# Kernel optimization log

Measured on AMD Instinct MI355X. Metric: run time of the kernel, lower is better.

The kernel has to match this reference:

```python
import jax, jax.numpy as jnp
import numpy as np

ALPHA = 0.9
DT = 0.1


def setup_inputs() -> dict:
    key = jax.random.key(0)
    ks = jax.random.split(key, 9)
    B, N_in, N, L, N_out, T = 256, 784, 1024, 4, 10, 100
    s = 0.05  # small init scale to keep sin() in a sensible regime
    return {
        "X": jax.random.normal(ks[0], (B, N_in), jnp.float32),
        "Wi_w": jax.random.normal(ks[1], (N, N_in), jnp.float32) * s,
        "Wi_b": jax.random.normal(ks[2], (N,), jnp.float32) * s,
        "Win_w": jax.random.normal(ks[3], (L, N, N), jnp.float32) * s,
        "Win_b": jax.random.normal(ks[4], (L, N), jnp.float32) * s,
        "Wrec_w": jax.random.normal(ks[5], (L, N, N), jnp.float32) * s,
        "Wrec_b": jax.random.normal(ks[6], (L, N), jnp.float32) * s,
        "Wo_w": jax.random.normal(ks[7], (N_out, N), jnp.float32) * s,
        "Wo_b": jax.random.normal(ks[8], (N_out,), jnp.float32) * s,
        "T": 100,
    }


def reference(X, Wi_w, Wi_b, Win_w, Win_b, Wrec_w, Wrec_b, Wo_w, Wo_b, T):
    L = Wrec_w.shape[0]
    B = X.shape[0]
    N = Wi_w.shape[0]
    # input projection computed once (as in the original: x_in outside the loop)
    x_in = X.reshape(B, -1) @ Wi_w.T + Wi_b  # [B, N]
    h0 = jnp.zeros((L, B, N), X.dtype)

    def step(h, _):
        hs = []
        # layer 0: dh = -alpha*h + sin(x_in + W_rec0 h)
        h0n = h[0] + DT * (-ALPHA * h[0] + jnp.sin(x_in + h[0] @ Wrec_w[0].T + Wrec_b[0]))
        hs.append(h0n)
        # layers 1..L-1 use the *updated* h of the layer below (matches torch loop order)
        for l in range(1, L):
            pre = hs[l - 1] @ Win_w[l].T + Win_b[l] + h[l] @ Wrec_w[l].T + Wrec_b[l]
            hs.append(h[l] + DT * (-ALPHA * h[l] + jnp.sin(pre)))
        return jnp.stack(hs), None

    hT, _ = jax.lax.scan(step, h0, None, length=T)
    return hT[-1] @ Wo_w.T + Wo_b  # [B, N_out]
```

## Files before the change

kernel.cpp:

```cpp
#include <hip/hip_runtime.h>
#include <hip/hip_fp16.h>

constexpr float ALPHA = 0.9f;
constexpr float DT    = 0.1f;
constexpr int BB   = 256;
constexpr int NIN  = 784;
constexpr int NN   = 1024;
constexpr int LL   = 4;
constexpr int NOUT = 10;
constexpr int TT   = 100;
constexpr int KXP  = 832;
constexpr int NSTAGE = TT + LL - 1;
constexpr unsigned GRIDN = 256;
constexpr unsigned GRPSZ = 32;
constexpr int NC = 32;

typedef _Float16 f16x8 __attribute__((ext_vector_type(8)));
typedef _Float16 f16x4 __attribute__((ext_vector_type(4)));
typedef float    f32x4 __attribute__((ext_vector_type(4)));

#define GLL16(g, l) __builtin_amdgcn_global_load_lds( \
    (const __attribute__((address_space(1))) unsigned int*)(g), \
    (__attribute__((address_space(3))) unsigned int*)(l), 16, 0, 0)

#define VMCNT(n) asm volatile("s_waitcnt vmcnt(" #n ")" ::: "memory")

__global__ void wconv_kernel(const float* __restrict__ Wrec,
                             const float* __restrict__ Win,
                             _Float16* __restrict__ Wrec_h,
                             _Float16* __restrict__ Win_h) {
    size_t i = (size_t)blockIdx.x * blockDim.x + threadIdx.x;
    float4 r = ((const float4*)Wrec)[i];
    float4 n = ((const float4*)Win)[i];
    f16x4 rh = {(_Float16)r.x, (_Float16)r.y, (_Float16)r.z, (_Float16)r.w};
    f16x4 nh = {(_Float16)n.x, (_Float16)n.y, (_Float16)n.z, (_Float16)n.w};
    ((f16x4*)Wrec_h)[i] = rh;
    ((f16x4*)Win_h)[i]  = nh;
}

__global__ void prep_kernel(const float* __restrict__ X,
                            const float* __restrict__ Wi_w,
                            _Float16* __restrict__ Xh_hi, _Float16* __restrict__ Xh_lo,
                            _Float16* __restrict__ Wih_hi, _Float16* __restrict__ Wih_lo) {
    int row = blockIdx.x;
    const float* src;
    _Float16 *dhi, *dlo;
    if (row < BB) {
        src = X + (size_t)row * NIN;
        dhi = Xh_hi + (size_t)row * KXP;  dlo = Xh_lo + (size_t)row * KXP;
    } else {
        int r = row - BB;
        src = Wi_w + (size_t)r * NIN;
        dhi = Wih_hi + (size_t)r * KXP;   dlo = Wih_lo + (size_t)r * KXP;
    }
    for (int k = threadIdx.x; k < KXP; k += 256) {
        float v = (k < NIN) ? src[k] : 0.f;
        _Float16 hi = (_Float16)v;
        dhi[k] = hi;
        dlo[k] = (_Float16)(v - (float)hi);
    }
}

__global__ void bias_kernel(const float* __restrict__ Win_b,
                            const float* __restrict__ Wrec_b,
                            float* __restrict__ bc) {
    int i = blockIdx.x * 256 + threadIdx.x;
    int l = i >> 10;
    float v = Wrec_b[i];
    if (l > 0) v += Win_b[i];
    bc[i] = v;
}

__global__ __launch_bounds__(256, 1) void xin_gemm(
    const _Float16* __restrict__ Xh_hi, const _Float16* __restrict__ Xh_lo,
    const _Float16* __restrict__ Wih_hi, const _Float16* __restrict__ Wih_lo,
    const float* __restrict__ Wi_b, float* __restrict__ x_in) {
    const int b = blockIdx.x;
    const int mt = b & 1, nt = b >> 1;
    const int row0 = mt * 128, col0 = nt * 64;

    const _Float16* Alist[3] = { Xh_hi + (size_t)row0 * KXP, Xh_hi + (size_t)row0 * KXP,
                                 Xh_lo + (size_t)row0 * KXP };
    const _Float16* Blist[3] = { Wih_hi + (size_t)col0 * KXP, Wih_lo + (size_t)col0 * KXP,
                                 Wih_hi + (size_t)col0 * KXP };

    __shared__ __align__(16) _Float16 ldsA[2][128 * 64];
    __shared__ __align__(16) _Float16 ldsB[2][64 * 64];

    const int tid = threadIdx.x;
    const int w = tid >> 6, lane = tid & 63;
    const int lm = lane & 15, kg = lane >> 4;
    const int rsub = lane >> 3, cch = lane & 7;
    const int wr = w >> 1, wc = w & 1;

    f32x4 acc[4][2] = {};
    constexpr int NIT = 3 * (KXP / 64);

    auto stage = [&](int kk, int buf) {
        int p = (kk >= 26) ? 2 : (kk >= 13 ? 1 : 0);
        int kw = (kk - p * 13) * 64;
        const _Float16* Ap = Alist[p];
        const _Float16* Bp = Blist[p];
        #pragma unroll
        for (int i = 0; i < 4; ++i) {
            const _Float16* g = Ap + (size_t)((w * 4 + i) * 8 + rsub) * KXP + kw + ((cch ^ rsub) * 8);
            GLL16(g, &ldsA[buf][(w * 4 + i) * 512]);
        }
        #pragma unroll
        for (int i = 0; i < 2; ++i) {
            const _Float16* g = Bp + (size_t)((w * 2 + i) * 8 + rsub) * KXP + kw + ((cch ^ rsub) * 8);
            GLL16(g, &ldsB[buf][(w * 2 + i) * 512]);
        }
    };

    stage(0, 0);
    __syncthreads();
    for (int kk = 0; kk < NIT; ++kk) {
        int cur = kk & 1;
        if (kk + 1 < NIT) stage(kk + 1, cur ^ 1);
        const _Float16* lA = ldsA[cur];
        const _Float16* lB = ldsB[cur];
        #pragma unroll
        for (int ks = 0; ks < 2; ++ks) {
            f16x8 a[4], bf[2];
            #pragma unroll
            for (int am = 0; am < 4; ++am) {
                int r = wr * 64 + am * 16 + lm;
                a[am] = *(const f16x8*)(lA + r * 64 + ((((ks << 2) | kg) ^ (lm & 7)) * 8));
            }
            #pragma unroll
            for (int bn = 0; bn < 2; ++bn) {
                int c = wc * 32 + bn * 16 + lm;
                bf[bn] = *(const f16x8*)(lB + c * 64 + ((((ks << 2) | kg) ^ (lm & 7)) * 8));
            }
            #pragma unroll
            for (int am = 0; am < 4; ++am)
                #pragma unroll
                for (int bn = 0; bn < 2; ++bn)
                    acc[am][bn] = __builtin_amdgcn_mfma_f32_16x16x32_f16(a[am], bf[bn], acc[am][bn], 0, 0, 0);
        }
        __syncthreads();
    }

    #pragma unroll
    for (int am = 0; am < 4; ++am)
        #pragma unroll
        for (int bn = 0; bn < 2; ++bn)
            #pragma unroll
            for (int r = 0; r < 4; ++r) {
                int row = row0 + wr * 64 + am * 16 + kg * 4 + r;
                int col = col0 + wc * 32 + bn * 16 + lm;
                x_in[(size_t)row * NN + col] = acc[am][bn][r] + Wi_b[col];
            }
}

__device__ __forceinline__ void grid_bar(unsigned* base) {
    __syncthreads();
    if (threadIdx.x == 0) {
        unsigned* flag = base + 15;
        unsigned pg = __hip_atomic_fetch_add(base + (blockIdx.x & 7), 1u,
                                             __ATOMIC_ACQ_REL, __HIP_MEMORY_SCOPE_AGENT);
        if (pg == GRPSZ - 1) {
            unsigned pr = __hip_atomic_fetch_add(base + 8, 1u,
                                                 __ATOMIC_ACQ_REL, __HIP_MEMORY_SCOPE_AGENT);
            if (pr == 7)
                __hip_atomic_store(flag, 1u, __ATOMIC_RELEASE, __HIP_MEMORY_SCOPE_AGENT);
        }
        for (int it = 0; it < (1 << 20); ++it) {
            if (__hip_atomic_load(flag, __ATOMIC_RELAXED, __HIP_MEMORY_SCOPE_AGENT)) break;
            __builtin_amdgcn_s_sleep(2);
        }
        (void)__hip_atomic_load(flag, __ATOMIC_ACQUIRE, __HIP_MEMORY_SCOPE_AGENT);
    }
    __syncthreads();
}

__global__ __launch_bounds__(512, 2) void persist_kernel(
    const _Float16* __restrict__ Wrec_h,
    const _Float16* __restrict__ Win_h,
    const float* __restrict__ bc,
    const float* __restrict__ x_in,
    float* __restrict__ Hf,
    _Float16* __restrict__ Hh,
    unsigned* __restrict__ bar) {
    const int b = blockIdx.x;
    const int l  = (b & 7) >> 1;
    const int mt = b & 1;
    const int nt = b >> 3;
    const int row0 = mt * 128, col0 = nt * 32;
    const size_t HSZ = (size_t)BB * NN;

    __shared__ __align__(16) _Float16 ldsW[2][NC][32][32];
    __shared__ __align__(16) _Float16 ldsA[3][8][16][32];

    const int tid = threadIdx.x;
    const int w = tid >> 6, lane = tid & 63;
    const int lm = lane & 15, kg = lane >> 4;

    {
        const int j   = tid & 3;
        const int col = (tid >> 2) & 31;
        const int pp  = tid >> 7;
        const int ng  = (l > 0) ? 2 : 1;
        for (int g = 0; g < ng; ++g) {
            const _Float16* Wg = (g ? Win_h : Wrec_h) + (size_t)l * NN * NN
                                 + (size_t)(col0 + col) * NN;
            #pragma unroll
            for (int q = 0; q < 8; ++q) {
                int chunk = pp * 8 + q;
                f16x8 v = *(const f16x8*)(Wg + chunk * 32 + ((j ^ (col & 3)) * 8));
                *(f16x8*)(&ldsW[g][chunk][col][j * 8]) = v;
            }
        }
    }

    float bias0 = bc[l * NN + col0 + lm];
    float bias1 = bc[l * NN + col0 + 16 + lm];
    float hreg[2][4] = {};
    float xin[2][4] = {};
    if (l == 0) {
        #pragma unroll
        for (int r = 0; r < 4; ++r) {
            int row = row0 + w * 16 + kg * 4 + r;
            xin[0][r] = x_in[(size_t)row * NN + col0 + lm];
            xin[1][r] = x_in[(size_t)row * NN + col0 + 16 + lm];
        }
    }
    __syncthreads();

    const int arow  = lane >> 2;
    const int aslot = (lane & 3) ^ (arow & 3);

    for (int s = 0; s < NSTAGE; ++s) {
        const int t = s - l;
        if (t >= 0 && t < TT) {
            const int src = t & 1, dst = src ^ 1;
            const _Float16* A0 = Hh + ((size_t)src * LL + l) * HSZ;
            const _Float16* A1 = (l > 0) ? Hh + ((size_t)dst * LL + (l - 1)) * HSZ : A0;
            f32x4 acc0 = {0.f, 0.f, 0.f, 0.f};
            f32x4 acc1 = {0.f, 0.f, 0.f, 0.f};
            const int ngem = (l > 0) ? 2 : 1;
            for (int g = 0; g < ngem; ++g) {
                const _Float16* Ap = (g ? A1 : A0)
                    + (size_t)(row0 + w * 16 + arow) * NN + aslot * 8;
                #define AISSUE(c, buf) GLL16(Ap + (c) * 32, &ldsA[buf][w][0][0])
                AISSUE(0, 0); AISSUE(1, 1);
                #pragma unroll
                for (int kk = 0; kk < NC; ++kk) {
                    if (kk < NC - 1) { VMCNT(1); } else { VMCNT(0); }
                    f16x8 a  = *(const f16x8*)(&ldsA[kk % 3][w][lm][(kg ^ (lm & 3)) * 8]);
                    f16x8 b0 = *(const f16x8*)(&ldsW[g][kk][lm][(kg ^ (lm & 3)) * 8]);
                    f16x8 b1 = *(const f16x8*)(&ldsW[g][kk][16 + lm][(kg ^ (lm & 3)) * 8]);
                    if (kk + 2 < NC) AISSUE(kk + 2, (kk + 2) % 3);
                    acc0 = __builtin_amdgcn_mfma_f32_16x16x32_f16(a, b0, acc0, 0, 0, 0);
                    acc1 = __builtin_amdgcn_mfma_f32_16x16x32_f16(a, b1, acc1, 0, 0, 0);
                }
                #undef AISSUE
            }
            _Float16* Hhd = Hh + ((size_t)dst * LL + l) * HSZ;
            #pragma unroll
            for (int r = 0; r < 4; ++r) {
                int row = row0 + w * 16 + kg * 4 + r;
                float pre0 = acc0[r] + bias0;
                float pre1 = acc1[r] + bias1;
                if (l == 0) { pre0 += xin[0][r]; pre1 += xin[1][r]; }
                float h0 = hreg[0][r];
                h0 = h0 + DT * (-ALPHA * h0 + __sinf(pre0));
                hreg[0][r] = h0;
                Hhd[(size_t)row * NN + col0 + lm] = (_Float16)h0;
                float h1 = hreg[1][r];
                h1 = h1 + DT * (-ALPHA * h1 + __sinf(pre1));
                hreg[1][r] = h1;
                Hhd[(size_t)row * NN + col0 + 16 + lm] = (_Float16)h1;
            }
        }
        if (s < NSTAGE - 1) grid_bar(bar + s * 16);
    }

    if (l == 3) {
        float* Hfl = Hf + (size_t)3 * HSZ;
        #pragma unroll
        for (int r = 0; r < 4; ++r) {
            int row = row0 + w * 16 + kg * 4 + r;
            Hfl[(size_t)row * NN + col0 + lm]      = hreg[0][r];
            Hfl[(size_t)row * NN + col0 + 16 + lm] = hreg[1][r];
        }
    }
}

__global__ __launch_bounds__(256) void out_kernel(
    const float* __restrict__ Hf, const float* __restrict__ Wo_w,
    const float* __restrict__ Wo_b, float* __restrict__ out) {
    const int r = blockIdx.x, tid = threadIdx.x;
    const int lane = tid & 63, w = tid >> 6;
    const float* h = Hf + (size_t)3 * BB * NN + (size_t)r * NN;
    float4 h4 = ((const float4*)h)[tid];
    __shared__ float red[4][16];
    #pragma unroll
    for (int jo = 0; jo < NOUT; ++jo) {
        float4 w4 = ((const float4*)(Wo_w + (size_t)jo * NN))[tid];
        float p = h4.x * w4.x + h4.y * w4.y + h4.z * w4.z + h4.w * w4.w;
        #pragma unroll
        for (int off = 32; off; off >>= 1) p += __shfl_down(p, off);
        if (lane == 0) red[w][jo] = p;
    }
    __syncthreads();
    if (tid < NOUT)
        out[r * NOUT + tid] = red[0][tid] + red[1][tid] + red[2][tid] + red[3][tid] + Wo_b[tid];
}

extern "C" void kernel_launch(void* const* d_in, const int* in_sizes, int n_in,
                              void* d_out, int out_size, void* d_ws, size_t ws_size,
                              hipStream_t stream) {
    const float* X      = (const float*)d_in[0];
    const float* Wi_w   = (const float*)d_in[1];
    const float* Wi_b   = (const float*)d_in[2];
    const float* Win_w  = (const float*)d_in[3];
    const float* Win_b  = (const float*)d_in[4];
    const float* Wrec_w = (const float*)d_in[5];
    const float* Wrec_b = (const float*)d_in[6];
    const float* Wo_w   = (const float*)d_in[7];
    const float* Wo_b   = (const float*)d_in[8];

    char* ws = (char*)d_ws;
    _Float16* Wrec_h = (_Float16*)(ws);
    _Float16* Win_h  = (_Float16*)(ws + (size_t)(8u  << 20));
    float*    Hf     = (float*)   (ws + (size_t)(16u << 20));
    _Float16* Hh     = (_Float16*)(ws + (size_t)(20u << 20));
    float*    x_in   = (float*)   (ws + (size_t)(24u << 20));
    float*    bc     = (float*)   (ws + (size_t)(25u << 20));
    _Float16* Xh_hi  = (_Float16*)(ws + (size_t)(25u << 20) + (64u << 10));
    _Float16* Xh_lo  = (_Float16*)(ws + (size_t)(25u << 20) + (576u << 10));
    unsigned* bar    = (unsigned*)(ws + (size_t)(26u << 20));
    _Float16* Wih_hi = (_Float16*)(ws + (size_t)(20u << 20));
    _Float16* Wih_lo = Wih_hi + (size_t)NN * KXP;

    wconv_kernel<<<4096, 256, 0, stream>>>(Wrec_w, Win_w, Wrec_h, Win_h);
    prep_kernel<<<BB + NN, 256, 0, stream>>>(X, Wi_w, Xh_hi, Xh_lo, Wih_hi, Wih_lo);
    bias_kernel<<<16, 256, 0, stream>>>(Win_b, Wrec_b, bc);
    xin_gemm<<<32, 256, 0, stream>>>(Xh_hi, Xh_lo, Wih_hi, Wih_lo, Wi_b, x_in);

    hipMemsetAsync(Hf, 0, (size_t)LL * BB * NN * sizeof(float), stream);
    hipMemsetAsync(Hh, 0, (size_t)2 * LL * BB * NN * sizeof(_Float16), stream);
    hipMemsetAsync(bar, 0, NSTAGE * 16 * sizeof(unsigned), stream);

    persist_kernel<<<GRIDN, 512, 0, stream>>>(Wrec_h, Win_h, bc, x_in, Hf, Hh, bar);

    out_kernel<<<BB, 256, 0, stream>>>(Hf, Wo_w, Wo_b, (float*)d_out);
}
```

Measured before the change: 2.427 ms.

## Rearrange LDS tiles k-slot-major and issue A prefetch before waiting

Changes the LDS layout of the weight and activation tiles from row-major with an XOR swizzle to a k-slot-major layout, so each MFMA operand read is a contiguous 16-byte slice per lane and needs no swizzle arithmetic. The global-to-LDS prefetch of chunk kk+2 is now issued before the vmcnt wait with a deeper count, which keeps more loads in flight. The spin barrier's sleep is shortened to reduce wake-up latency. The new layout may change LDS bank-conflict behaviour, and the earlier issue of the prefetch writes a buffer slot whose previous contents must already have been consumed.

```diff
diff --git a/kernel.cpp b/kernel.cpp
--- a/kernel.cpp
+++ b/kernel.cpp
@@ -13,7 +13,7 @@
 constexpr int NSTAGE = TT + LL - 1;
 constexpr unsigned GRIDN = 256;
 constexpr unsigned GRPSZ = 32;
-constexpr int NC = 32;
+constexpr int NCH = 32;
 
 typedef _Float16 f16x8 __attribute__((ext_vector_type(8)));
 typedef _Float16 f16x4 __attribute__((ext_vector_type(4)));
@@ -168,7 +168,7 @@
         }
         for (int it = 0; it < (1 << 20); ++it) {
             if (__hip_atomic_load(flag, __ATOMIC_RELAXED, __HIP_MEMORY_SCOPE_AGENT)) break;
-            __builtin_amdgcn_s_sleep(2);
+            __builtin_amdgcn_s_sleep(1);
         }
         (void)__hip_atomic_load(flag, __ATOMIC_ACQUIRE, __HIP_MEMORY_SCOPE_AGENT);
     }
@@ -190,26 +190,26 @@
     const int row0 = mt * 128, col0 = nt * 32;
     const size_t HSZ = (size_t)BB * NN;
 
-    __shared__ __align__(16) _Float16 ldsW[2][NC][32][32];
-    __shared__ __align__(16) _Float16 ldsA[3][8][16][32];
+    __shared__ __align__(16) _Float16 ldsW[2][NCH][4][32][8];
+    __shared__ __align__(16) _Float16 ldsA[3][8][4][16][8];
 
     const int tid = threadIdx.x;
     const int w = tid >> 6, lane = tid & 63;
     const int lm = lane & 15, kg = lane >> 4;
 
     {
-        const int j   = tid & 3;
-        const int col = (tid >> 2) & 31;
-        const int pp  = tid >> 7;
-        const int ng  = (l > 0) ? 2 : 1;
+        const int ng = (l > 0) ? 2 : 1;
         for (int g = 0; g < ng; ++g) {
             const _Float16* Wg = (g ? Win_h : Wrec_h) + (size_t)l * NN * NN
-                                 + (size_t)(col0 + col) * NN;
+                                 + (size_t)col0 * NN;
             #pragma unroll
             for (int q = 0; q < 8; ++q) {
-                int chunk = pp * 8 + q;
-                f16x8 v = *(const f16x8*)(Wg + chunk * 32 + ((j ^ (col & 3)) * 8));
-                *(f16x8*)(&ldsW[g][chunk][col][j * 8]) = v;
+                int idx = q * 512 + tid;
+                int col = idx >> 7;
+                int c   = (idx >> 2) & 31;
+                int sl  = idx & 3;
+                f16x8 v = *(const f16x8*)(Wg + (size_t)col * NN + c * 32 + sl * 8);
+                *(f16x8*)&ldsW[g][c][sl][col][0] = v;
             }
         }
     }
@@ -227,9 +227,6 @@
         }
     }
     __syncthreads();
-
-    const int arow  = lane >> 2;
-    const int aslot = (lane & 3) ^ (arow & 3);
 
     for (int s = 0; s < NSTAGE; ++s) {
         const int t = s - l;
@@ -242,20 +239,21 @@
             const int ngem = (l > 0) ? 2 : 1;
             for (int g = 0; g < ngem; ++g) {
                 const _Float16* Ap = (g ? A1 : A0)
-                    + (size_t)(row0 + w * 16 + arow) * NN + aslot * 8;
-                #define AISSUE(c, buf) GLL16(Ap + (c) * 32, &ldsA[buf][w][0][0])
-                AISSUE(0, 0); AISSUE(1, 1);
+                    + (size_t)(row0 + w * 16 + lm) * NN + kg * 8;
+                #define AISS(c, buf) GLL16(Ap + (c) * 32, &ldsA[buf][w][0][0][0])
+                AISS(0, 0); AISS(1, 1);
                 #pragma unroll
-                for (int kk = 0; kk < NC; ++kk) {
-                    if (kk < NC - 1) { VMCNT(1); } else { VMCNT(0); }
-                    f16x8 a  = *(const f16x8*)(&ldsA[kk % 3][w][lm][(kg ^ (lm & 3)) * 8]);
-                    f16x8 b0 = *(const f16x8*)(&ldsW[g][kk][lm][(kg ^ (lm & 3)) * 8]);
-                    f16x8 b1 = *(const f16x8*)(&ldsW[g][kk][16 + lm][(kg ^ (lm & 3)) * 8]);
-                    if (kk + 2 < NC) AISSUE(kk + 2, (kk + 2) % 3);
+                for (int kk = 0; kk < NCH; ++kk) {
+                    if (kk + 2 < NCH) { AISS(kk + 2, (kk + 2) % 3); VMCNT(2); }
+                    else if (kk + 1 < NCH) { VMCNT(1); }
+                    else { VMCNT(0); }
+                    f16x8 a  = *(const f16x8*)&ldsA[kk % 3][w][kg][lm][0];
+                    f16x8 b0 = *(const f16x8*)&ldsW[g][kk][kg][lm][0];
+                    f16x8 b1 = *(const f16x8*)&ldsW[g][kk][kg][lm + 16][0];
                     acc0 = __builtin_amdgcn_mfma_f32_16x16x32_f16(a, b0, acc0, 0, 0, 0);
                     acc1 = __builtin_amdgcn_mfma_f32_16x16x32_f16(a, b1, acc1, 0, 0, 0);
                 }
-                #undef AISSUE
+                #undef AISS
             }
             _Float16* Hhd = Hh + ((size_t)dst * LL + l) * HSZ;
             #pragma unroll
```

New measurement: 2.782 ms. 14.6% more time.
